# Performance work log

Hardware: AMD Instinct MI355X
Metric: run time of the kernel (lower is better)

The kernel has to match this reference:

```python
import jax, jax.numpy as jnp
import numpy as np

B, S, H, D = 4, 4096, 8, 128
EPS = 1e-6


def layernorm(x, g, b, axes):
    m = jnp.mean(x, axis=axes, keepdims=True)
    v = jnp.mean(jnp.square(x - m), axis=axes, keepdims=True)
    return (x - m) / jnp.sqrt(v + EPS) * g + b


def setup_inputs() -> dict:
    key = jax.random.key(0)
    ks = jax.random.split(key, 6)
    scale = 0.05
    return {
        "heads_input": jax.random.normal(ks[0], (B, S, H, D), jnp.float32),
        # GroupLinear trans_hid: per-head (2D -> 3D)
        "W_hid": jax.random.normal(ks[1], (H, 2 * D, 3 * D), jnp.float32) * scale,
        "b_hid": jax.random.normal(ks[2], (H, 3 * D), jnp.float32) * scale,
        # GroupLinear trans_og: per-head (2D -> D)
        "W_og": jax.random.normal(ks[3], (H, 2 * D, D), jnp.float32) * scale,
        "b_og": jax.random.normal(ks[4], (H, D), jnp.float32) * scale,
        # LayerNorm affine params (elementwise_affine=True)
        "ln_csum_g": jnp.ones((H, D), jnp.float32),
        "ln_csum_b": jnp.zeros((H, D), jnp.float32),
        "ln_hid_g": jnp.ones((H, 3, D), jnp.float32),
        "ln_hid_b": jnp.zeros((H, 3, D), jnp.float32),
        "ln_og_g": jnp.ones((H, D), jnp.float32),
        "ln_og_b": jnp.zeros((H, D), jnp.float32),
        "init_cx": jnp.zeros((1, H, D), jnp.float32),
    }


def reference(heads_input, W_hid, b_hid, W_og, b_og, ln_csum_g, ln_csum_b,
              ln_hid_g, ln_hid_b, ln_og_g, ln_og_b, init_cx):
    b, s, h, d = heads_input.shape
    # shifted cumulative sum over time, then LayerNorm over (head, dim)
    shifted = jnp.concatenate(
        [jnp.zeros((b, 1, h, d), heads_input.dtype), heads_input[:, :-1]], axis=1)
    csum = layernorm(jnp.cumsum(shifted, axis=1), ln_csum_g, ln_csum_b, (-2, -1))
    cat = jnp.concatenate([heads_input, csum], axis=-1)        # [b,s,h,2d]
    hid = jnp.einsum('bshi,hio->bsho', cat, W_hid) + b_hid     # [b,s,h,3d]
    hid = layernorm(hid.reshape(b, s, h, 3, d), ln_hid_g, ln_hid_b, (-3, -2, -1))
    igate, fgate, hidden = hid[..., 0, :], hid[..., 1, :], hid[..., 2, :]
    fgate = jax.nn.sigmoid(fgate)
    igh = jax.nn.sigmoid(igate) * jax.nn.relu(hidden)
    # LGateFunc: cell_t = fgate_t * cell_{t-1} + igh_t, cell_0 = init_cx
    c0 = jnp.broadcast_to(init_cx, (b, h, d)).astype(heads_input.dtype)
    def step(c, fi):
        f, i = fi
        c = f * c + i
        return c, c
    _, cells = jax.lax.scan(step, c0,
                            (fgate.transpose(1, 0, 2, 3), igh.transpose(1, 0, 2, 3)))
    cell = cells.transpose(1, 0, 2, 3)                          # [b,s,h,d]
    og_in = jnp.concatenate([heads_input, cell], axis=-1)       # [b,s,h,2d]
    og = layernorm(jnp.einsum('bshi,hio->bsho', og_in, W_og) + b_og,
                   ln_og_g, ln_og_b, (-2, -1))
    return jax.nn.sigmoid(og) * cell
```

## Files before the change

kernel.cpp:

```cpp
#include <hip/hip_runtime.h>

#define EPSF 1e-6f


typedef __attribute__((ext_vector_type(8))) short short8v;
typedef __attribute__((ext_vector_type(4))) float float4v;

__device__ __forceinline__ float sigm(float x) { return 1.0f / (1.0f + __expf(-x)); }

__device__ __forceinline__ unsigned short f2bf(float f) {
    unsigned int u = __float_as_uint(f);
    u = (u + 0x7fffu + ((u >> 16) & 1u)) >> 16;
    return (unsigned short)u;
}
__device__ __forceinline__ float bf2f(unsigned short s) { return __uint_as_float(((unsigned int)s) << 16); }
__device__ __forceinline__ float bf2f_lo(unsigned int p) { return __uint_as_float(p << 16); }
__device__ __forceinline__ float bf2f_hi(unsigned int p) { return __uint_as_float(p & 0xffff0000u); }
__device__ __forceinline__ unsigned int pack2bf(float a, float b) {
    return (unsigned int)f2bf(a) | ((unsigned int)f2bf(b) << 16);
}

__device__ __forceinline__ void block_reduce2(float& a, float& b) {
#pragma unroll
    for (int off = 32; off > 0; off >>= 1) {
        a += __shfl_down(a, off);
        b += __shfl_down(b, off);
    }
    __shared__ float sa[8], sb[8];
    int wid = threadIdx.x >> 6;
    int lane = threadIdx.x & 63;
    if (lane == 0) { sa[wid] = a; sb[wid] = b; }
    __syncthreads();
    a = sa[0] + sa[1] + sa[2] + sa[3];
    b = sb[0] + sb[1] + sb[2] + sb[3];
}

__global__ __launch_bounds__(256) void k_prep_w(const float* __restrict__ W, unsigned short* __restrict__ Wt,
                                                int Nw) {
    int idx = blockIdx.x * 256 + threadIdx.x;
    int k = idx & 255;
    int rest = idx >> 8;
    int o = rest % Nw;
    int h = rest / Nw;
    Wt[idx] = f2bf(W[((size_t)h * 256 + k) * Nw + o]);
}

__global__ __launch_bounds__(256) void k_cumsum_a(const float* __restrict__ X, float* __restrict__ cS,
                                                  unsigned short* __restrict__ XB) {
    int t = blockIdx.x * 256 + threadIdx.x;
    int d = t & 127, h = (t >> 7) & 7, k = (t >> 10) & 63, b = t >> 16;
    size_t base = (((size_t)(b * 4096 + k * 64)) * 8 + h) * 128 + d;
    float s = 0.f;
    for (int j = 0; j < 64; ++j) {
        unsigned short xb = f2bf(X[base + (size_t)j * 1024]);
        XB[base + (size_t)j * 1024] = xb;
        s += bf2f(xb);
    }
    cS[(size_t)((b * 8 + h) * 128 + d) * 64 + k] = s;
}

__global__ __launch_bounds__(256) void k_cumsum_b(const float* __restrict__ cS, float* __restrict__ cO) {
    int wave = (blockIdx.x * 256 + threadIdx.x) >> 6;
    int lane = threadIdx.x & 63;
    size_t idx = (size_t)wave * 64 + lane;
    float v = cS[idx];
    float incl = v;
#pragma unroll
    for (int d = 1; d < 64; d <<= 1) {
        float t = __shfl_up(incl, d);
        if (lane >= d) incl += t;
    }
    cO[idx] = incl - v;
}

__global__ __launch_bounds__(256) void k_cumsum_c(const unsigned short* __restrict__ XB,
                                                  const float* __restrict__ cO,
                                                  unsigned short* __restrict__ CSUMB) {
    int t = blockIdx.x * 256 + threadIdx.x;
    int d = t & 127, h = (t >> 7) & 7, k = (t >> 10) & 63, b = t >> 16;
    int ch = (b * 8 + h) * 128 + d;
    float run = cO[(size_t)ch * 64 + k];
    size_t base = (((size_t)(b * 4096 + k * 64)) * 8 + h) * 128 + d;
    for (int j = 0; j < 64; ++j) {
        float x = bf2f(XB[base + (size_t)j * 1024]);
        CSUMB[base + (size_t)j * 1024] = f2bf(run);
        run += x;
    }
}

__global__ __launch_bounds__(256) void k_ln_csum(const unsigned short* __restrict__ CSUMB,
                                                 unsigned short* __restrict__ CSB,
                                                 const float* __restrict__ g, const float* __restrict__ bb) {
    int bs = blockIdx.x, t = threadIdx.x;
    uint2 u = ((const uint2*)(CSUMB + (size_t)bs * 1024))[t];
    float4 v;
    v.x = bf2f_lo(u.x); v.y = bf2f_hi(u.x);
    v.z = bf2f_lo(u.y); v.w = bf2f_hi(u.y);
    float s = v.x + v.y + v.z + v.w;
    float ss = v.x * v.x + v.y * v.y + v.z * v.z + v.w * v.w;
    block_reduce2(s, ss);
    float m = s * (1.f / 1024.f);
    float var = ss * (1.f / 1024.f) - m * m;
    float r = rsqrtf(fmaxf(var, 0.f) + EPSF);
    float4 gv = ((const float4*)g)[t];
    float4 bv = ((const float4*)bb)[t];
    uint2 o;
    o.x = pack2bf((v.x - m) * r * gv.x + bv.x, (v.y - m) * r * gv.y + bv.y);
    o.y = pack2bf((v.z - m) * r * gv.z + bv.z, (v.w - m) * r * gv.w + bv.w);
    ((uint2*)(CSB + (size_t)bs * 1024))[t] = o;
}

__global__ __launch_bounds__(512) void k_gemm_bf16(const unsigned short* __restrict__ A1,
                                                   const unsigned short* __restrict__ A2,
                                                   const unsigned short* __restrict__ Wt,
                                                   const float* __restrict__ bias,
                                                   unsigned short* __restrict__ OUT, int Nw, int m0,
                                                   int nbx) {
    __shared__ short As[4][8192];
    __shared__ short Bs[4][8192];
    int bid = blockIdx.x;
    int h = bid & 7;
    int rest = bid >> 3;
    int bx = rest % nbx;
    int by = rest / nbx;
    int t0 = threadIdx.x;
    int lane = t0 & 63, wid = t0 >> 6;
    int wr = wid >> 1, wc = wid & 1;
    int l15 = lane & 15, l4 = lane >> 4;
    int lr = lane >> 3, lc = lane & 7;
    const int bxc = bx * 128;
    const size_t mbase = (size_t)(m0 + by * 128);

    float4v acc[2][4];
#pragma unroll
    for (int i = 0; i < 2; ++i)
#pragma unroll
        for (int j = 0; j < 4; ++j) acc[i][j] = (float4v)(0.f);

    auto STAGE = [&](int t) {
        const unsigned short* src = (t < 2) ? A1 : A2;
        int kofs = (t & 1) * 64;
#pragma unroll
        for (int it = 0; it < 2; ++it) {
            int r0 = wid * 16 + it * 8;
            int r = r0 + lr;
            int c = lc ^ (r & 7);
            size_t g = ((mbase + r) * 8 + h) * 128 + kofs + c * 8;
            __builtin_amdgcn_global_load_lds((const __attribute__((address_space(1))) void*)(src + g),
                                             (__attribute__((address_space(3))) void*)(&As[t][r0 * 64]),
                                             16, 0, 0);
        }
#pragma unroll
        for (int it = 0; it < 2; ++it) {
            int n0 = wid * 16 + it * 8;
            int cl = n0 + lr;
            int c = lc ^ (cl & 7);
            size_t g = ((size_t)(h * Nw + bxc + cl)) * 256 + t * 64 + c * 8;
            __builtin_amdgcn_global_load_lds((const __attribute__((address_space(1))) void*)(Wt + g),
                                             (__attribute__((address_space(3))) void*)(&Bs[t][n0 * 64]),
                                             16, 0, 0);
        }
    };

    STAGE(0); STAGE(1); STAGE(2); STAGE(3);

#pragma unroll
    for (int t = 0; t < 4; ++t) {
        if (t == 0)      asm volatile("s_waitcnt vmcnt(12)" ::: "memory");
        else if (t == 1) asm volatile("s_waitcnt vmcnt(8)" ::: "memory");
        else if (t == 2) asm volatile("s_waitcnt vmcnt(4)" ::: "memory");
        else             asm volatile("s_waitcnt vmcnt(0)" ::: "memory");
        __builtin_amdgcn_s_barrier();
        __builtin_amdgcn_sched_barrier(0);
#pragma unroll
        for (int kk = 0; kk < 2; ++kk) {
            short8v a[2], b[4];
#pragma unroll
            for (int i = 0; i < 2; ++i) {
                int r = wr * 32 + i * 16 + l15;
                int slot = (kk * 4 + l4) ^ (r & 7);
                a[i] = *(const short8v*)(&As[t][r * 64 + slot * 8]);
            }
#pragma unroll
            for (int j = 0; j < 4; ++j) {
                int c = wc * 64 + j * 16 + l15;
                int slot = (kk * 4 + l4) ^ (c & 7);
                b[j] = *(const short8v*)(&Bs[t][c * 64 + slot * 8]);
            }
#pragma unroll
            for (int i = 0; i < 2; ++i)
#pragma unroll
                for (int j = 0; j < 4; ++j)
                    acc[i][j] = __builtin_amdgcn_mfma_f32_16x16x32_bf16(a[i], b[j], acc[i][j], 0, 0, 0);
        }
    }
#pragma unroll
    for (int j = 0; j < 4; ++j) {
        int o = bxc + wc * 64 + j * 16 + l15;
        float bv = bias[h * Nw + o];
#pragma unroll
        for (int i = 0; i < 2; ++i) {
            int mlb = by * 128 + wr * 32 + i * 16 + l4 * 4;
#pragma unroll
            for (int q = 0; q < 4; ++q) {
                OUT[((size_t)(mlb + q) * 8 + h) * Nw + o] = f2bf(acc[i][j][q] + bv);
            }
        }
    }
}

__global__ __launch_bounds__(256) void k_ln_gates(const unsigned short* __restrict__ HID,
                                                  unsigned short* __restrict__ FG,
                                                  unsigned short* __restrict__ IG,
                                                  const float* __restrict__ g, const float* __restrict__ bb,
                                                  int m0) {
    __shared__ float sm[3072];
    int bsl = blockIdx.x, t = threadIdx.x;
    int bs = m0 + bsl;
    const uint4* row = (const uint4*)(HID + (size_t)bsl * 3072);
    float s = 0.f, ss = 0.f;
    for (int idx = t; idx < 384; idx += 256) {
        uint4 u = row[idx];
        float f0 = bf2f_lo(u.x), f1 = bf2f_hi(u.x);
        float f2 = bf2f_lo(u.y), f3 = bf2f_hi(u.y);
        float f4 = bf2f_lo(u.z), f5 = bf2f_hi(u.z);
        float f6 = bf2f_lo(u.w), f7 = bf2f_hi(u.w);
        float* p = sm + idx * 8;
        p[0] = f0; p[1] = f1; p[2] = f2; p[3] = f3; p[4] = f4; p[5] = f5; p[6] = f6; p[7] = f7;
        s += f0 + f1 + f2 + f3 + f4 + f5 + f6 + f7;
        ss += f0 * f0 + f1 * f1 + f2 * f2 + f3 * f3 + f4 * f4 + f5 * f5 + f6 * f6 + f7 * f7;
    }
    block_reduce2(s, ss);
    float m = s * (1.f / 3072.f);
    float var = ss * (1.f / 3072.f) - m * m;
    float r = rsqrtf(fmaxf(var, 0.f) + EPSF);
    int u0 = t * 4;
    int h = u0 >> 7;
    int d0 = u0 & 127;
    float fr[4], ir[4];
#pragma unroll
    for (int q = 0; q < 4; ++q) {
        int d = d0 + q;
        float yi = sm[h * 384 + d];
        float yf = sm[h * 384 + 128 + d];
        float yh = sm[h * 384 + 256 + d];
        float ni = (yi - m) * r * g[(h * 3 + 0) * 128 + d] + bb[(h * 3 + 0) * 128 + d];
        float nf = (yf - m) * r * g[(h * 3 + 1) * 128 + d] + bb[(h * 3 + 1) * 128 + d];
        float nh = (yh - m) * r * g[(h * 3 + 2) * 128 + d] + bb[(h * 3 + 2) * 128 + d];
        fr[q] = sigm(nf);
        ir[q] = sigm(ni) * fmaxf(nh, 0.f);
    }
    uint2 fo, io;
    fo.x = pack2bf(fr[0], fr[1]); fo.y = pack2bf(fr[2], fr[3]);
    io.x = pack2bf(ir[0], ir[1]); io.y = pack2bf(ir[2], ir[3]);
    ((uint2*)(FG + (size_t)bs * 1024))[t] = fo;
    ((uint2*)(IG + (size_t)bs * 1024))[t] = io;
}

__global__ __launch_bounds__(256) void k_scan_a(const unsigned short* __restrict__ FG,
                                                const unsigned short* __restrict__ IG,
                                                float* __restrict__ cF, float* __restrict__ cC) {
    int t = blockIdx.x * 256 + threadIdx.x;
    int d2 = t & 63, h = (t >> 6) & 7, k = (t >> 9) & 63, b = t >> 15;
    size_t base = (((size_t)(b * 4096 + k * 64)) * 8 + h) * 64 + d2;
    const unsigned int* FGu = (const unsigned int*)FG;
    const unsigned int* IGu = (const unsigned int*)IG;
    float F0 = 1.f, C0 = 0.f, F1 = 1.f, C1 = 0.f;
    for (int j = 0; j < 64; ++j) {
        unsigned int fg = FGu[base + (size_t)j * 512];
        unsigned int ig = IGu[base + (size_t)j * 512];
        float f0 = bf2f_lo(fg), f1 = bf2f_hi(fg);
        C0 = fmaf(f0, C0, bf2f_lo(ig)); F0 *= f0;
        C1 = fmaf(f1, C1, bf2f_hi(ig)); F1 *= f1;
    }
    size_t ci0 = ((size_t)((b * 8 + h) * 128 + d2 * 2)) * 64 + k;
    cF[ci0] = F0; cC[ci0] = C0;
    cF[ci0 + 64] = F1; cC[ci0 + 64] = C1;
}

__global__ __launch_bounds__(256) void k_scan_b(const float* __restrict__ cF, const float* __restrict__ cC,
                                                const float* __restrict__ initcx, float* __restrict__ cI) {
    int wave = (blockIdx.x * 256 + threadIdx.x) >> 6;
    int lane = threadIdx.x & 63;
    size_t idx = (size_t)wave * 64 + lane;
    float F = cF[idx], C = cC[idx];
#pragma unroll
    for (int d = 1; d < 64; d <<= 1) {
        float Fp = __shfl_up(F, d);
        float Cp = __shfl_up(C, d);
        if (lane >= d) { C = fmaf(Cp, F, C); F *= Fp; }
    }
    float Fe = __shfl_up(F, 1);
    float Ce = __shfl_up(C, 1);
    if (lane == 0) { Fe = 1.f; Ce = 0.f; }
    float c0 = initcx[wave & 1023];
    cI[idx] = fmaf(Fe, c0, Ce);
}

__global__ __launch_bounds__(256) void k_scan_c(const unsigned short* __restrict__ FG,
                                                unsigned short* __restrict__ IGCLB,
                                                const float* __restrict__ cI) {
    int t = blockIdx.x * 256 + threadIdx.x;
    int d2 = t & 63, h = (t >> 6) & 7, k = (t >> 9) & 63, b = t >> 15;
    size_t base = (((size_t)(b * 4096 + k * 64)) * 8 + h) * 64 + d2;
    const unsigned int* FGu = (const unsigned int*)FG;
    unsigned int* IGu = (unsigned int*)IGCLB;
    size_t ci0 = ((size_t)((b * 8 + h) * 128 + d2 * 2)) * 64 + k;
    float c0 = cI[ci0], c1 = cI[ci0 + 64];
    for (int j = 0; j < 64; ++j) {
        unsigned int fg = FGu[base + (size_t)j * 512];
        unsigned int ig = IGu[base + (size_t)j * 512];
        c0 = fmaf(bf2f_lo(fg), c0, bf2f_lo(ig));
        c1 = fmaf(bf2f_hi(fg), c1, bf2f_hi(ig));
        IGu[base + (size_t)j * 512] = pack2bf(c0, c1);
    }
}

__global__ __launch_bounds__(256) void k_ln_out(const unsigned short* __restrict__ OG,
                                                const unsigned short* __restrict__ CLB,
                                                const float* __restrict__ g, const float* __restrict__ bb,
                                                float* __restrict__ OUT, int m0) {
    int bsl = blockIdx.x, t = threadIdx.x;
    int bs = m0 + bsl;
    uint2 u = ((const uint2*)(OG + (size_t)bsl * 1024))[t];
    float4 v;
    v.x = bf2f_lo(u.x); v.y = bf2f_hi(u.x);
    v.z = bf2f_lo(u.y); v.w = bf2f_hi(u.y);
    float s = v.x + v.y + v.z + v.w;
    float ss = v.x * v.x + v.y * v.y + v.z * v.z + v.w * v.w;
    block_reduce2(s, ss);
    float m = s * (1.f / 1024.f);
    float var = ss * (1.f / 1024.f) - m * m;
    float r = rsqrtf(fmaxf(var, 0.f) + EPSF);
    float4 gv = ((const float4*)g)[t];
    float4 bv = ((const float4*)bb)[t];
    uint2 cu = ((const uint2*)(CLB + (size_t)bs * 1024))[t];
    float4 cv;
    cv.x = bf2f_lo(cu.x); cv.y = bf2f_hi(cu.x);
    cv.z = bf2f_lo(cu.y); cv.w = bf2f_hi(cu.y);
    float4 o;
    o.x = sigm((v.x - m) * r * gv.x + bv.x) * cv.x;
    o.y = sigm((v.y - m) * r * gv.y + bv.y) * cv.y;
    o.z = sigm((v.z - m) * r * gv.z + bv.z) * cv.z;
    o.w = sigm((v.w - m) * r * gv.w + bv.w) * cv.w;
    ((float4*)(OUT + (size_t)bs * 1024))[t] = o;
}

extern "C" void kernel_launch(void* const* d_in, const int* in_sizes, int n_in,
                              void* d_out, int out_size, void* d_ws, size_t ws_size,
                              hipStream_t stream) {
    const float* X      = (const float*)d_in[0];
    const float* W_hid  = (const float*)d_in[1];
    const float* b_hid  = (const float*)d_in[2];
    const float* W_og   = (const float*)d_in[3];
    const float* b_og   = (const float*)d_in[4];
    const float* g_cs   = (const float*)d_in[5];
    const float* b_cs   = (const float*)d_in[6];
    const float* g_hid  = (const float*)d_in[7];
    const float* b_hidl = (const float*)d_in[8];
    const float* g_og   = (const float*)d_in[9];
    const float* b_ogl  = (const float*)d_in[10];
    const float* initcx = (const float*)d_in[11];

    float* ws = (float*)d_ws;
    const size_t O_SC    = 0ull;
    const size_t O_XB    = 1310720ull;
    const size_t O_CSUMB = 9699328ull;
    const size_t O_CSB   = 18087936ull;
    const size_t O_IGB   = 26476544ull;
    const size_t O_WTH   = 34865152ull;
    const size_t O_WTO   = 35258368ull;
    const size_t O_HID   = 35389440ull;

    float* cS = ws + O_SC;
    float* cO = cS + 262144;
    float* cF = cO + 262144;
    float* cC = cF + 262144;
    float* cI = cC + 262144;
    unsigned short* XB    = (unsigned short*)(ws + O_XB);
    unsigned short* CSUMB = (unsigned short*)(ws + O_CSUMB);
    unsigned short* FGB   = CSUMB;
    unsigned short* CSB   = (unsigned short*)(ws + O_CSB);
    unsigned short* IGB   = (unsigned short*)(ws + O_IGB);
    unsigned short* CLB   = IGB;
    unsigned short* WTH   = (unsigned short*)(ws + O_WTH);
    unsigned short* WTO   = (unsigned short*)(ws + O_WTO);
    unsigned short* HIDC  = (unsigned short*)(ws + O_HID);

    size_t avail = (ws_size / 4 > O_HID) ? ws_size / 4 - O_HID : 0;
    int CH = 1024;
    for (int c = 16384; c >= 1024; c >>= 1) {
        if ((size_t)c * 1536ull <= avail) { CH = c; break; }
    }
    const int NC = 16384 / CH;

    dim3 blk(256);
    dim3 blkg(512);
    k_prep_w<<<3072, blk, 0, stream>>>(W_hid, WTH, 384);
    k_prep_w<<<1024, blk, 0, stream>>>(W_og, WTO, 128);
    k_cumsum_a<<<1024, blk, 0, stream>>>(X, cS, XB);
    k_cumsum_b<<<1024, blk, 0, stream>>>(cS, cO);
    k_cumsum_c<<<1024, blk, 0, stream>>>(XB, cO, CSUMB);
    k_ln_csum<<<16384, blk, 0, stream>>>(CSUMB, CSB, g_cs, b_cs);
    for (int c = 0; c < NC; ++c) {
        int m0 = c * CH;
        k_gemm_bf16<<<8 * 3 * (CH / 128), blkg, 0, stream>>>(XB, CSB, WTH, b_hid, HIDC, 384, m0, 3);
        k_ln_gates<<<CH, blk, 0, stream>>>(HIDC, FGB, IGB, g_hid, b_hidl, m0);
    }
    k_scan_a<<<512, blk, 0, stream>>>(FGB, IGB, cF, cC);
    k_scan_b<<<1024, blk, 0, stream>>>(cF, cC, initcx, cI);
    k_scan_c<<<512, blk, 0, stream>>>(FGB, IGB, cI);
    for (int c = 0; c < NC; ++c) {
        int m0 = c * CH;
        k_gemm_bf16<<<8 * 1 * (CH / 128), blkg, 0, stream>>>(XB, CLB, WTO, b_og, HIDC, 128, m0, 1);
        k_ln_out<<<CH, blk, 0, stream>>>(HIDC, CLB, g_og, b_ogl, (float*)d_out, m0);
    }
}
```

Measured before the change: 242.5 us.

## Store GEMM A-operands in head-major planar layout for contiguous row loads

New measurement: 254.4 us. +4.9%, slower.

```diff
diff --git a/kernel.cpp b/kernel.cpp
--- a/kernel.cpp
+++ b/kernel.cpp
@@ -49,11 +49,12 @@
                                                   unsigned short* __restrict__ XB) {
     int t = blockIdx.x * 256 + threadIdx.x;
     int d = t & 127, h = (t >> 7) & 7, k = (t >> 10) & 63, b = t >> 16;
-    size_t base = (((size_t)(b * 4096 + k * 64)) * 8 + h) * 128 + d;
+    size_t xbase = (((size_t)(b * 4096 + k * 64)) * 8 + h) * 128 + d;
+    size_t pbase = ((size_t)h * 16384 + b * 4096 + k * 64) * 128 + d;
     float s = 0.f;
     for (int j = 0; j < 64; ++j) {
-        unsigned short xb = f2bf(X[base + (size_t)j * 1024]);
-        XB[base + (size_t)j * 1024] = xb;
+        unsigned short xb = f2bf(X[xbase + (size_t)j * 1024]);
+        XB[pbase + (size_t)j * 128] = xb;
         s += bf2f(xb);
     }
     cS[(size_t)((b * 8 + h) * 128 + d) * 64 + k] = s;
@@ -80,10 +81,10 @@
     int d = t & 127, h = (t >> 7) & 7, k = (t >> 10) & 63, b = t >> 16;
     int ch = (b * 8 + h) * 128 + d;
     float run = cO[(size_t)ch * 64 + k];
-    size_t base = (((size_t)(b * 4096 + k * 64)) * 8 + h) * 128 + d;
+    size_t pbase = ((size_t)h * 16384 + b * 4096 + k * 64) * 128 + d;
     for (int j = 0; j < 64; ++j) {
-        float x = bf2f(XB[base + (size_t)j * 1024]);
-        CSUMB[base + (size_t)j * 1024] = f2bf(run);
+        float x = bf2f(XB[pbase + (size_t)j * 128]);
+        CSUMB[pbase + (size_t)j * 128] = f2bf(run);
         run += x;
     }
 }
@@ -92,7 +93,9 @@
                                                  unsigned short* __restrict__ CSB,
                                                  const float* __restrict__ g, const float* __restrict__ bb) {
     int bs = blockIdx.x, t = threadIdx.x;
-    uint2 u = ((const uint2*)(CSUMB + (size_t)bs * 1024))[t];
+    int h = t >> 5, c = t & 31;
+    size_t u2i = ((size_t)h * 16384 + bs) * 32 + c;
+    uint2 u = ((const uint2*)CSUMB)[u2i];
     float4 v;
     v.x = bf2f_lo(u.x); v.y = bf2f_hi(u.x);
     v.z = bf2f_lo(u.y); v.w = bf2f_hi(u.y);
@@ -107,7 +110,7 @@
     uint2 o;
     o.x = pack2bf((v.x - m) * r * gv.x + bv.x, (v.y - m) * r * gv.y + bv.y);
     o.y = pack2bf((v.z - m) * r * gv.z + bv.z, (v.w - m) * r * gv.w + bv.w);
-    ((uint2*)(CSB + (size_t)bs * 1024))[t] = o;
+    ((uint2*)CSB)[u2i] = o;
 }
 
 __global__ __launch_bounds__(512) void k_gemm_bf16(const unsigned short* __restrict__ A1,
@@ -130,6 +133,7 @@
     int lr = lane >> 3, lc = lane & 7;
     const int bxc = bx * 128;
     const size_t mbase = (size_t)(m0 + by * 128);
+    const size_t aplane = (size_t)h * 16384;
 
     float4v acc[2][4];
 #pragma unroll
@@ -145,7 +149,7 @@
             int r0 = wid * 16 + it * 8;
             int r = r0 + lr;
             int c = lc ^ (r & 7);
-            size_t g = ((mbase + r) * 8 + h) * 128 + kofs + c * 8;
+            size_t g = (aplane + mbase + r) * 128 + kofs + c * 8;
             __builtin_amdgcn_global_load_lds((const __attribute__((address_space(1))) void*)(src + g),
                                              (__attribute__((address_space(3))) void*)(&As[t][r0 * 64]),
                                              16, 0, 0);
@@ -298,13 +302,16 @@
 }
 
 __global__ __launch_bounds__(256) void k_scan_c(const unsigned short* __restrict__ FG,
-                                                unsigned short* __restrict__ IGCLB,
+                                                const unsigned short* __restrict__ IG,
+                                                unsigned short* __restrict__ CLB,
                                                 const float* __restrict__ cI) {
     int t = blockIdx.x * 256 + threadIdx.x;
     int d2 = t & 63, h = (t >> 6) & 7, k = (t >> 9) & 63, b = t >> 15;
     size_t base = (((size_t)(b * 4096 + k * 64)) * 8 + h) * 64 + d2;
+    size_t pbase = ((size_t)h * 16384 + b * 4096 + k * 64) * 64 + d2;
     const unsigned int* FGu = (const unsigned int*)FG;
-    unsigned int* IGu = (unsigned int*)IGCLB;
+    const unsigned int* IGu = (const unsigned int*)IG;
+    unsigned int* CLu = (unsigned int*)CLB;
     size_t ci0 = ((size_t)((b * 8 + h) * 128 + d2 * 2)) * 64 + k;
     float c0 = cI[ci0], c1 = cI[ci0 + 64];
     for (int j = 0; j < 64; ++j) {
@@ -312,7 +319,7 @@
         unsigned int ig = IGu[base + (size_t)j * 512];
         c0 = fmaf(bf2f_lo(fg), c0, bf2f_lo(ig));
         c1 = fmaf(bf2f_hi(fg), c1, bf2f_hi(ig));
-        IGu[base + (size_t)j * 512] = pack2bf(c0, c1);
+        CLu[pbase + (size_t)j * 64] = pack2bf(c0, c1);
     }
 }
 
@@ -334,7 +341,8 @@
     float r = rsqrtf(fmaxf(var, 0.f) + EPSF);
     float4 gv = ((const float4*)g)[t];
     float4 bv = ((const float4*)bb)[t];
-    uint2 cu = ((const uint2*)(CLB + (size_t)bs * 1024))[t];
+    int h = t >> 5, c = t & 31;
+    uint2 cu = ((const uint2*)CLB)[((size_t)h * 16384 + bs) * 32 + c];
     float4 cv;
     cv.x = bf2f_lo(cu.x); cv.y = bf2f_hi(cu.x);
     cv.z = bf2f_lo(cu.y); cv.w = bf2f_hi(cu.y);
@@ -368,9 +376,10 @@
     const size_t O_CSUMB = 9699328ull;
     const size_t O_CSB   = 18087936ull;
     const size_t O_IGB   = 26476544ull;
-    const size_t O_WTH   = 34865152ull;
-    const size_t O_WTO   = 35258368ull;
-    const size_t O_HID   = 35389440ull;
+    const size_t O_CLB   = 34865152ull;
+    const size_t O_WTH   = 43253760ull;
+    const size_t O_WTO   = 43646976ull;
+    const size_t O_HID   = 43778048ull;
 
     float* cS = ws + O_SC;
     float* cO = cS + 262144;
@@ -382,7 +391,7 @@
     unsigned short* FGB   = CSUMB;
     unsigned short* CSB   = (unsigned short*)(ws + O_CSB);
     unsigned short* IGB   = (unsigned short*)(ws + O_IGB);
-    unsigned short* CLB   = IGB;
+    unsigned short* CLB   = (unsigned short*)(ws + O_CLB);
     unsigned short* WTH   = (unsigned short*)(ws + O_WTH);
     unsigned short* WTO   = (unsigned short*)(ws + O_WTO);
     unsigned short* HIDC  = (unsigned short*)(ws + O_HID);
@@ -409,7 +418,7 @@
     }
     k_scan_a<<<512, blk, 0, stream>>>(FGB, IGB, cF, cC);
     k_scan_b<<<1024, blk, 0, stream>>>(cF, cC, initcx, cI);
-    k_scan_c<<<512, blk, 0, stream>>>(FGB, IGB, cI);
+    k_scan_c<<<512, blk, 0, stream>>>(FGB, IGB, CLB, cI);
     for (int c = 0; c < NC; ++c) {
         int m0 = c * CH;
         k_gemm_bf16<<<8 * 1 * (CH / 128), blkg, 0, stream>>>(XB, CLB, WTO, b_og, HIDC, 128, m0, 1);
```
